# Performance work log

Hardware: AMD Instinct MI355X
Metric: run time of the kernel (lower is better)

Reference implementation:

```python
import jax, jax.numpy as jnp
import numpy as np

N, IN, OUT, T = 131072, 256, 256, 8

def setup_inputs() -> dict:
    key = jax.random.key(0)
    k1, k2, k3, k4 = jax.random.split(key, 4)
    x = jax.random.normal(k1, (N, IN), dtype=jnp.float32)
    type_vec = jnp.sort(jax.random.randint(k2, (N,), 0, T, dtype=jnp.int64))
    weight = jax.random.normal(k3, (T, IN, OUT), dtype=jnp.float32) * (1.0 / np.sqrt(IN))
    bias = jax.random.normal(k4, (T, OUT), dtype=jnp.float32) * 0.01
    return {"x": x, "type_vec": type_vec, "weight": weight, "bias": bias}

def reference(x, type_vec, weight, bias):
    # HeteroLinear fused forward: out[i] = x[i] @ weight[type_vec[i]] + bias[type_vec[i]]
    # Loop over the small fixed set of types (T=8); mask-accumulate keeps memory at O(N*OUT).
    num_types = weight.shape[0]
    out = jnp.zeros((x.shape[0], weight.shape[2]), dtype=x.dtype)
    for t in range(num_types):
        mask = (type_vec == t)[:, None]  # [N,1]
        out = out + jnp.where(mask, x @ weight[t] + bias[t], jnp.zeros((), x.dtype))
    return out
```

## Files before the change

kernel.cpp:

```cpp
#include <hip/hip_runtime.h>
#include <hip/hip_bf16.h>


#define NROWS 131072
#define KD 256
#define ND 256
#define BM 256
#define NBLK (NROWS / BM)

typedef __attribute__((ext_vector_type(8))) short short8;
typedef __attribute__((ext_vector_type(4))) float f32x4;
typedef __attribute__((ext_vector_type(4))) float flt4;

typedef __attribute__((address_space(3))) unsigned int lds_u32_t;
typedef __attribute__((address_space(1))) unsigned int glb_u32_t;

__device__ inline unsigned short f2bf(float f) {
    unsigned int u = __float_as_uint(f);
    u += 0x7FFFu + ((u >> 16) & 1u);
    return (unsigned short)(u >> 16);
}

__global__ __launch_bounds__(256) void prep_weights(const float* __restrict__ w,
                                                    unsigned short* __restrict__ wT) {
    __shared__ unsigned short L[8][264];
    const int t  = blockIdx.x >> 5;
    const int k0 = (blockIdx.x & 31) * 8;
    const int tid = threadIdx.x;

    #pragma unroll
    for (int i = 0; i < 2; ++i) {
        int idx = i * 256 + tid;
        int kr  = idx >> 6;
        int nq  = idx & 63;
        const flt4* src = (const flt4*)(w + ((size_t)t * 256 + k0 + kr) * 256);
        flt4 v = src[nq];
        #pragma unroll
        for (int j = 0; j < 4; ++j) L[kr][nq * 4 + j] = f2bf(v[j]);
    }
    __syncthreads();

    int n = tid;
    short8 v;
    #pragma unroll
    for (int j = 0; j < 8; ++j) v[j] = (short)L[j][n];
    *(short8*)(wT + ((size_t)t * 256 + n) * 256 + k0) = v;
}

__global__ __launch_bounds__(512) void hetero_gemm(
        const float* __restrict__ x, const int* __restrict__ tv,
        const unsigned short* __restrict__ wT, const float* __restrict__ bias,
        float* __restrict__ out) {
    __shared__ short Bs[BM * KD];

    const int tid  = threadIdx.x;
    const int lane = tid & 63;
    const int wv   = tid >> 6;
    const int cl   = lane & 15;
    const int kg   = lane >> 4;
    const int r0   = blockIdx.x * BM;
    const int rw   = r0 + wv * 32;

    const int tmin = tv[r0];
    const int tmax = tv[r0 + BM - 1];
    const int ty0  = tv[rw + cl];
    const int ty1  = tv[rw + 16 + cl];
    const int s    = cl & 7;

    const float* xr0 = x + (size_t)(rw + cl) * KD + kg * 8;
    const float* xr1 = x + (size_t)(rw + 16 + cl) * KD + kg * 8;

    for (int t = tmin; t <= tmax; ++t) {
        if (t > tmin) __syncthreads();

        {
            const unsigned short* Wt = wT + (size_t)t * (KD * ND);
            #pragma unroll
            for (int rnd = 0; rnd < 16; ++rnd) {
                int i   = rnd * 512 + tid;
                int col = i >> 5;
                int c   = i & 31;
                int sc  = c ^ (col & 7);
                const unsigned short* gp = Wt + col * KD + sc * 8;
                __builtin_amdgcn_global_load_lds(
                    (const glb_u32_t*)gp,
                    (lds_u32_t*)((char*)Bs + (size_t)(rnd * 512 + wv * 64) * 16),
                    16, 0, 0);
            }
        }
        __syncthreads();

        #pragma unroll
        for (int half = 0; half < 2; ++half) {
            const int c0 = half * 128;

            f32x4 zero = {0.f, 0.f, 0.f, 0.f};
            f32x4 acc[2][8];
            #pragma unroll
            for (int m = 0; m < 2; ++m)
                #pragma unroll
                for (int n = 0; n < 8; ++n) acc[m][n] = zero;

            f32x4 xbA[4], xbB[4];
            xbA[0] = *(const f32x4*)(xr0);
            xbA[1] = *(const f32x4*)(xr0 + 4);
            xbA[2] = *(const f32x4*)(xr1);
            xbA[3] = *(const f32x4*)(xr1 + 4);
            xbB[0] = *(const f32x4*)(xr0 + 32);
            xbB[1] = *(const f32x4*)(xr0 + 36);
            xbB[2] = *(const f32x4*)(xr1 + 32);
            xbB[3] = *(const f32x4*)(xr1 + 36);

            auto step = [&](f32x4 (&xb)[4], int ks) {
                short8 a[2];
                #pragma unroll
                for (int m = 0; m < 2; ++m) {
                    #pragma unroll
                    for (int j = 0; j < 4; ++j) {
                        a[m][j]     = (short)f2bf(xb[2 * m][j]);
                        a[m][4 + j] = (short)f2bf(xb[2 * m + 1][j]);
                    }
                }
                if (ks + 2 < 8) {
                    xb[0] = *(const f32x4*)(xr0 + (ks + 2) * 32);
                    xb[1] = *(const f32x4*)(xr0 + (ks + 2) * 32 + 4);
                    xb[2] = *(const f32x4*)(xr1 + (ks + 2) * 32);
                    xb[3] = *(const f32x4*)(xr1 + (ks + 2) * 32 + 4);
                }
                #pragma unroll
                for (int n = 0; n < 8; ++n) {
                    int lc = c0 + n * 16 + cl;
                    int kc = ((ks << 2) | kg) ^ s;
                    short8 b = *(const short8*)((char*)Bs + (size_t)lc * 512 + (kc << 4));
                    acc[0][n] = __builtin_amdgcn_mfma_f32_16x16x32_bf16(b, a[0], acc[0][n], 0, 0, 0);
                    acc[1][n] = __builtin_amdgcn_mfma_f32_16x16x32_bf16(b, a[1], acc[1][n], 0, 0, 0);
                }
            };
            step(xbA, 0); step(xbB, 1); step(xbA, 2); step(xbB, 3);
            step(xbA, 4); step(xbB, 5); step(xbA, 6); step(xbB, 7);

            #pragma unroll
            for (int m = 0; m < 2; ++m) {
                int tym = (m == 0) ? ty0 : ty1;
                if (tym == t) {
                    float* orow = out + (size_t)(rw + m * 16 + cl) * ND + c0 + kg * 4;
                    #pragma unroll
                    for (int n = 0; n < 8; ++n) {
                        f32x4 bv = *(const f32x4*)(bias + (size_t)t * ND + c0 + n * 16 + kg * 4);
                        *(f32x4*)(orow + n * 16) = acc[m][n] + bv;
                    }
                }
            }
        }
    }
}

extern "C" void kernel_launch(void* const* d_in, const int* in_sizes, int n_in,
                              void* d_out, int out_size, void* d_ws, size_t ws_size,
                              hipStream_t stream) {
    const float* x    = (const float*)d_in[0];
    const int*   tv   = (const int*)d_in[1];
    const float* w    = (const float*)d_in[2];
    const float* bias = (const float*)d_in[3];
    float* out = (float*)d_out;
    unsigned short* wT = (unsigned short*)d_ws;

    prep_weights<<<dim3(256), dim3(256), 0, stream>>>(w, wT);
    hetero_gemm<<<dim3(NBLK), dim3(512), 0, stream>>>(x, tv, wT, bias, out);
}
```

Baseline: 66.80 us.

## Split output columns across workgroups with 128-row tiles and swizzled block mapping

Each workgroup now covers 128 rows and one 128-column half of the output with 4 waves, instead of 256 rows and both halves with 8 waves. The LDS weight tile drops to 64KB, so more workgroups can be resident per CU. A blockIdx remap spreads neighbouring row groups across XCDs. The bf16 conversion now uses the library intrinsic. The trade-off is that each x row is read and converted twice, once per column half, and weight tiles are reloaded more often overall.

New measurement: 91.09 us. 36.4% more time.

```diff
diff --git a/kernel.cpp b/kernel.cpp
--- a/kernel.cpp
+++ b/kernel.cpp
@@ -5,8 +5,9 @@
 #define NROWS 131072
 #define KD 256
 #define ND 256
-#define BM 256
-#define NBLK (NROWS / BM)
+#define BR 128
+#define NRG (NROWS / BR)
+#define NBLK (NRG * 2)
 
 typedef __attribute__((ext_vector_type(8))) short short8;
 typedef __attribute__((ext_vector_type(4))) float f32x4;
@@ -16,9 +17,7 @@
 typedef __attribute__((address_space(1))) unsigned int glb_u32_t;
 
 __device__ inline unsigned short f2bf(float f) {
-    unsigned int u = __float_as_uint(f);
-    u += 0x7FFFu + ((u >> 16) & 1u);
-    return (unsigned short)(u >> 16);
+    return __bfloat16_as_ushort(__float2bfloat16(f));
 }
 
 __global__ __launch_bounds__(256) void prep_weights(const float* __restrict__ w,
@@ -47,22 +46,25 @@
     *(short8*)(wT + ((size_t)t * 256 + n) * 256 + k0) = v;
 }
 
-__global__ __launch_bounds__(512) void hetero_gemm(
+__global__ __launch_bounds__(256) void hetero_gemm(
         const float* __restrict__ x, const int* __restrict__ tv,
         const unsigned short* __restrict__ wT, const float* __restrict__ bias,
         float* __restrict__ out) {
-    __shared__ short Bs[BM * KD];
+    __shared__ short Bs[128 * KD];
 
     const int tid  = threadIdx.x;
     const int lane = tid & 63;
     const int wv   = tid >> 6;
     const int cl   = lane & 15;
     const int kg   = lane >> 4;
-    const int r0   = blockIdx.x * BM;
+    const int wgid = (blockIdx.x & 7) * (NBLK / 8) + (blockIdx.x >> 3);
+    const int rg   = wgid >> 1;
+    const int c0   = (wgid & 1) * 128;
+    const int r0   = rg * BR;
     const int rw   = r0 + wv * 32;
 
     const int tmin = tv[r0];
-    const int tmax = tv[r0 + BM - 1];
+    const int tmax = tv[r0 + BR - 1];
     const int ty0  = tv[rw + cl];
     const int ty1  = tv[rw + 16 + cl];
     const int s    = cl & 7;
@@ -77,78 +79,73 @@
             const unsigned short* Wt = wT + (size_t)t * (KD * ND);
             #pragma unroll
             for (int rnd = 0; rnd < 16; ++rnd) {
-                int i   = rnd * 512 + tid;
-                int col = i >> 5;
+                int i   = rnd * 256 + tid;
+                int lc  = i >> 5;
                 int c   = i & 31;
-                int sc  = c ^ (col & 7);
-                const unsigned short* gp = Wt + col * KD + sc * 8;
+                int sc  = c ^ (lc & 7);
+                const unsigned short* gp = Wt + (size_t)(c0 + lc) * KD + sc * 8;
                 __builtin_amdgcn_global_load_lds(
                     (const glb_u32_t*)gp,
-                    (lds_u32_t*)((char*)Bs + (size_t)(rnd * 512 + wv * 64) * 16),
+                    (lds_u32_t*)((char*)Bs + (size_t)(rnd * 256 + wv * 64) * 16),
                     16, 0, 0);
             }
         }
         __syncthreads();
 
+        f32x4 zero = {0.f, 0.f, 0.f, 0.f};
+        f32x4 acc[2][8];
         #pragma unroll
-        for (int half = 0; half < 2; ++half) {
-            const int c0 = half * 128;
+        for (int m = 0; m < 2; ++m)
+            #pragma unroll
+            for (int n = 0; n < 8; ++n) acc[m][n] = zero;
 
-            f32x4 zero = {0.f, 0.f, 0.f, 0.f};
-            f32x4 acc[2][8];
+        f32x4 xbA[4], xbB[4];
+        xbA[0] = *(const f32x4*)(xr0);
+        xbA[1] = *(const f32x4*)(xr0 + 4);
+        xbA[2] = *(const f32x4*)(xr1);
+        xbA[3] = *(const f32x4*)(xr1 + 4);
+        xbB[0] = *(const f32x4*)(xr0 + 32);
+        xbB[1] = *(const f32x4*)(xr0 + 36);
+        xbB[2] = *(const f32x4*)(xr1 + 32);
+        xbB[3] = *(const f32x4*)(xr1 + 36);
+
+        auto step = [&](f32x4 (&xb)[4], int ks) {
+            short8 a[2];
             #pragma unroll
-            for (int m = 0; m < 2; ++m)
+            for (int m = 0; m < 2; ++m) {
                 #pragma unroll
-                for (int n = 0; n < 8; ++n) acc[m][n] = zero;
+                for (int j = 0; j < 4; ++j) {
+                    a[m][j]     = (short)f2bf(xb[2 * m][j]);
+                    a[m][4 + j] = (short)f2bf(xb[2 * m + 1][j]);
+                }
+            }
+            if (ks + 2 < 8) {
+                xb[0] = *(const f32x4*)(xr0 + (ks + 2) * 32);
+                xb[1] = *(const f32x4*)(xr0 + (ks + 2) * 32 + 4);
+                xb[2] = *(const f32x4*)(xr1 + (ks + 2) * 32);
+                xb[3] = *(const f32x4*)(xr1 + (ks + 2) * 32 + 4);
+            }
+            #pragma unroll
+            for (int n = 0; n < 8; ++n) {
+                int lc = n * 16 + cl;
+                int kc = ((ks << 2) | kg) ^ s;
+                short8 b = *(const short8*)((char*)Bs + (size_t)lc * 512 + (kc << 4));
+                acc[0][n] = __builtin_amdgcn_mfma_f32_16x16x32_bf16(b, a[0], acc[0][n], 0, 0, 0);
+                acc[1][n] = __builtin_amdgcn_mfma_f32_16x16x32_bf16(b, a[1], acc[1][n], 0, 0, 0);
+            }
+        };
+        step(xbA, 0); step(xbB, 1); step(xbA, 2); step(xbB, 3);
+        step(xbA, 4); step(xbB, 5); step(xbA, 6); step(xbB, 7);
 
-            f32x4 xbA[4], xbB[4];
-            xbA[0] = *(const f32x4*)(xr0);
-            xbA[1] = *(const f32x4*)(xr0 + 4);
-            xbA[2] = *(const f32x4*)(xr1);
-            xbA[3] = *(const f32x4*)(xr1 + 4);
-            xbB[0] = *(const f32x4*)(xr0 + 32);
-            xbB[1] = *(const f32x4*)(xr0 + 36);
-            xbB[2] = *(const f32x4*)(xr1 + 32);
-            xbB[3] = *(const f32x4*)(xr1 + 36);
-
-            auto step = [&](f32x4 (&xb)[4], int ks) {
-                short8 a[2];
-                #pragma unroll
-                for (int m = 0; m < 2; ++m) {
-                    #pragma unroll
-                    for (int j = 0; j < 4; ++j) {
-                        a[m][j]     = (short)f2bf(xb[2 * m][j]);
-                        a[m][4 + j] = (short)f2bf(xb[2 * m + 1][j]);
-                    }
-                }
-                if (ks + 2 < 8) {
-                    xb[0] = *(const f32x4*)(xr0 + (ks + 2) * 32);
-                    xb[1] = *(const f32x4*)(xr0 + (ks + 2) * 32 + 4);
-                    xb[2] = *(const f32x4*)(xr1 + (ks + 2) * 32);
-                    xb[3] = *(const f32x4*)(xr1 + (ks + 2) * 32 + 4);
-                }
+        #pragma unroll
+        for (int m = 0; m < 2; ++m) {
+            int tym = (m == 0) ? ty0 : ty1;
+            if (tym == t) {
+                float* orow = out + (size_t)(rw + m * 16 + cl) * ND + c0 + kg * 4;
                 #pragma unroll
                 for (int n = 0; n < 8; ++n) {
-                    int lc = c0 + n * 16 + cl;
-                    int kc = ((ks << 2) | kg) ^ s;
-                    short8 b = *(const short8*)((char*)Bs + (size_t)lc * 512 + (kc << 4));
-                    acc[0][n] = __builtin_amdgcn_mfma_f32_16x16x32_bf16(b, a[0], acc[0][n], 0, 0, 0);
-                    acc[1][n] = __builtin_amdgcn_mfma_f32_16x16x32_bf16(b, a[1], acc[1][n], 0, 0, 0);
-                }
-            };
-            step(xbA, 0); step(xbB, 1); step(xbA, 2); step(xbB, 3);
-            step(xbA, 4); step(xbB, 5); step(xbA, 6); step(xbB, 7);
-
-            #pragma unroll
-            for (int m = 0; m < 2; ++m) {
-                int tym = (m == 0) ? ty0 : ty1;
-                if (tym == t) {
-                    float* orow = out + (size_t)(rw + m * 16 + cl) * ND + c0 + kg * 4;
-                    #pragma unroll
-                    for (int n = 0; n < 8; ++n) {
-                        f32x4 bv = *(const f32x4*)(bias + (size_t)t * ND + c0 + n * 16 + kg * 4);
-                        *(f32x4*)(orow + n * 16) = acc[m][n] + bv;
-                    }
+                    f32x4 bv = *(const f32x4*)(bias + (size_t)t * ND + c0 + n * 16 + kg * 4);
+                    *(f32x4*)(orow + n * 16) = acc[m][n] + bv;
                 }
             }
         }
@@ -166,5 +163,5 @@
     unsigned short* wT = (unsigned short*)d_ws;
 
     prep_weights<<<dim3(256), dim3(256), 0, stream>>>(w, wT);
-    hetero_gemm<<<dim3(NBLK), dim3(512), 0, stream>>>(x, tv, wT, bias, out);
+    hetero_gemm<<<dim3(NBLK), dim3(256), 0, stream>>>(x, tv, wT, bias, out);
 }
```

## Split output columns across blocks and stage x tiles in LDS via async DMA

Applied to the files above, without the earlier changes.

Doubles the grid so each block computes one 128-column half of the output for its 256-row group, halving the weight tile kept in LDS. The x rows are now loaded with global_load_lds into a double-buffered, XOR-swizzled LDS area, using explicit vmcnt/lgkmcnt waits to overlap the next k-step's loads with the MFMAs. Block indices are remapped so that blocks sharing a row group are spread across XCDs. This is meant to raise occupancy and hide the latency of x loads. In exchange, every row of x is read twice from global memory, and the code depends on hand-written waitcnt and inline asm being correct.

New measurement: 69.86 us. 4.6% more time.

```diff
diff --git a/kernel.cpp b/kernel.cpp
--- a/kernel.cpp
+++ b/kernel.cpp
@@ -6,7 +6,7 @@
 #define KD 256
 #define ND 256
 #define BM 256
-#define NBLK (NROWS / BM)
+#define NBLK ((NROWS / BM) * 2)
 
 typedef __attribute__((ext_vector_type(8))) short short8;
 typedef __attribute__((ext_vector_type(4))) float f32x4;
@@ -19,6 +19,12 @@
     unsigned int u = __float_as_uint(f);
     u += 0x7FFFu + ((u >> 16) & 1u);
     return (unsigned short)(u >> 16);
+}
+
+__device__ inline f32x4 lds_read_b128(unsigned addr) {
+    f32x4 v;
+    asm volatile("ds_read_b128 %0, %1" : "=v"(v) : "v"(addr));
+    return v;
 }
 
 __global__ __launch_bounds__(256) void prep_weights(const float* __restrict__ w,
@@ -51,14 +57,18 @@
         const float* __restrict__ x, const int* __restrict__ tv,
         const unsigned short* __restrict__ wT, const float* __restrict__ bias,
         float* __restrict__ out) {
-    __shared__ short Bs[BM * KD];
+    __shared__ short Bs[128 * KD];
+    __shared__ float Xs[2 * 8 * 32 * 32];
 
     const int tid  = threadIdx.x;
     const int lane = tid & 63;
     const int wv   = tid >> 6;
     const int cl   = lane & 15;
     const int kg   = lane >> 4;
-    const int r0   = blockIdx.x * BM;
+    const int wgid = (blockIdx.x & 7) * (NBLK / 8) + (blockIdx.x >> 3);
+    const int rg   = wgid >> 1;
+    const int c0   = (wgid & 1) * 128;
+    const int r0   = rg * BM;
     const int rw   = r0 + wv * 32;
 
     const int tmin = tv[r0];
@@ -67,8 +77,20 @@
     const int ty1  = tv[rw + 16 + cl];
     const int s    = cl & 7;
 
-    const float* xr0 = x + (size_t)(rw + cl) * KD + kg * 8;
-    const float* xr1 = x + (size_t)(rw + 16 + cl) * KD + kg * 8;
+    const unsigned xwbase = (unsigned)(uintptr_t)&Xs[wv * 1024];
+
+    auto DMA_X = [&](int ks) {
+        const int buf = ks & 1;
+        #pragma unroll
+        for (int i = 0; i < 4; ++i) {
+            const float* gp = x + (size_t)(rw + 8 * i + (lane >> 3)) * KD
+                                + ks * 32 + (((lane & 7) ^ (lane >> 3)) << 2);
+            __builtin_amdgcn_global_load_lds(
+                (const glb_u32_t*)gp,
+                (lds_u32_t*)&Xs[(buf * 8 + wv) * 1024 + i * 256],
+                16, 0, 0);
+        }
+    };
 
     for (int t = tmin; t <= tmax; ++t) {
         if (t > tmin) __syncthreads();
@@ -76,79 +98,71 @@
         {
             const unsigned short* Wt = wT + (size_t)t * (KD * ND);
             #pragma unroll
-            for (int rnd = 0; rnd < 16; ++rnd) {
-                int i   = rnd * 512 + tid;
-                int col = i >> 5;
-                int c   = i & 31;
-                int sc  = c ^ (col & 7);
-                const unsigned short* gp = Wt + col * KD + sc * 8;
+            for (int rnd = 0; rnd < 8; ++rnd) {
+                int i  = rnd * 512 + tid;
+                int lc = i >> 5;
+                int c  = i & 31;
+                int sc = c ^ (lc & 7);
+                const unsigned short* gp = Wt + (size_t)(c0 + lc) * KD + sc * 8;
                 __builtin_amdgcn_global_load_lds(
                     (const glb_u32_t*)gp,
                     (lds_u32_t*)((char*)Bs + (size_t)(rnd * 512 + wv * 64) * 16),
                     16, 0, 0);
             }
         }
+        DMA_X(0); DMA_X(1);
         __syncthreads();
 
+        f32x4 zero = {0.f, 0.f, 0.f, 0.f};
+        f32x4 acc[2][8];
         #pragma unroll
-        for (int half = 0; half < 2; ++half) {
-            const int c0 = half * 128;
+        for (int m = 0; m < 2; ++m)
+            #pragma unroll
+            for (int n = 0; n < 8; ++n) acc[m][n] = zero;
 
-            f32x4 zero = {0.f, 0.f, 0.f, 0.f};
-            f32x4 acc[2][8];
-            #pragma unroll
-            for (int m = 0; m < 2; ++m)
-                #pragma unroll
-                for (int n = 0; n < 8; ++n) acc[m][n] = zero;
+        #define KSTEP(ks)                                                          \
+        {                                                                          \
+            if ((ks) < 7) asm volatile("s_waitcnt vmcnt(4)" ::: "memory");         \
+            else          asm volatile("s_waitcnt vmcnt(0)" ::: "memory");         \
+            __builtin_amdgcn_sched_barrier(0);                                     \
+            const unsigned sb = xwbase + (((ks) & 1) << 15);                       \
+            f32x4 v00 = lds_read_b128(sb + cl * 128 + (((2 * kg + 0) ^ s) << 4));  \
+            f32x4 v01 = lds_read_b128(sb + cl * 128 + (((2 * kg + 1) ^ s) << 4));  \
+            f32x4 v10 = lds_read_b128(sb + (16 + cl) * 128 + (((2 * kg + 0) ^ s) << 4)); \
+            f32x4 v11 = lds_read_b128(sb + (16 + cl) * 128 + (((2 * kg + 1) ^ s) << 4)); \
+            asm volatile("s_waitcnt lgkmcnt(0)" ::: "memory");                     \
+            __builtin_amdgcn_sched_barrier(0);                                     \
+            if ((ks) < 6) DMA_X((ks) + 2);           \
+            short8 a0, a1;                                                         \
+            _Pragma("unroll")                                                      \
+            for (int j = 0; j < 4; ++j) {                                          \
+                a0[j]     = (short)f2bf(v00[j]);                                   \
+                a0[4 + j] = (short)f2bf(v01[j]);                                   \
+                a1[j]     = (short)f2bf(v10[j]);                                   \
+                a1[4 + j] = (short)f2bf(v11[j]);                                   \
+            }                                                                      \
+            _Pragma("unroll")                                                      \
+            for (int n = 0; n < 8; ++n) {                                          \
+                int lc = n * 16 + cl;                                              \
+                int kc = (((ks) << 2) | kg) ^ s;                                   \
+                short8 b = *(const short8*)((char*)Bs + (size_t)lc * 512 + (kc << 4)); \
+                acc[0][n] = __builtin_amdgcn_mfma_f32_16x16x32_bf16(b, a0, acc[0][n], 0, 0, 0); \
+                acc[1][n] = __builtin_amdgcn_mfma_f32_16x16x32_bf16(b, a1, acc[1][n], 0, 0, 0); \
+            }                                                                      \
+        }
+        KSTEP(0) KSTEP(1) KSTEP(2) KSTEP(3)
+        KSTEP(4) KSTEP(5) KSTEP(6) KSTEP(7)
+        #undef KSTEP
 
-            f32x4 xbA[4], xbB[4];
-            xbA[0] = *(const f32x4*)(xr0);
-            xbA[1] = *(const f32x4*)(xr0 + 4);
-            xbA[2] = *(const f32x4*)(xr1);
-            xbA[3] = *(const f32x4*)(xr1 + 4);
-            xbB[0] = *(const f32x4*)(xr0 + 32);
-            xbB[1] = *(const f32x4*)(xr0 + 36);
-            xbB[2] = *(const f32x4*)(xr1 + 32);
-            xbB[3] = *(const f32x4*)(xr1 + 36);
-
-            auto step = [&](f32x4 (&xb)[4], int ks) {
-                short8 a[2];
-                #pragma unroll
-                for (int m = 0; m < 2; ++m) {
-                    #pragma unroll
-                    for (int j = 0; j < 4; ++j) {
-                        a[m][j]     = (short)f2bf(xb[2 * m][j]);
-                        a[m][4 + j] = (short)f2bf(xb[2 * m + 1][j]);
-                    }
-                }
-                if (ks + 2 < 8) {
-                    xb[0] = *(const f32x4*)(xr0 + (ks + 2) * 32);
-                    xb[1] = *(const f32x4*)(xr0 + (ks + 2) * 32 + 4);
-                    xb[2] = *(const f32x4*)(xr1 + (ks + 2) * 32);
-                    xb[3] = *(const f32x4*)(xr1 + (ks + 2) * 32 + 4);
-                }
+        #pragma unroll
+        for (int m = 0; m < 2; ++m) {
+            int tym = (m == 0) ? ty0 : ty1;
+            if (tym == t) {
+                float* orow = out + (size_t)(rw + m * 16 + cl) * ND + c0 + kg * 4;
                 #pragma unroll
                 for (int n = 0; n < 8; ++n) {
-                    int lc = c0 + n * 16 + cl;
-                    int kc = ((ks << 2) | kg) ^ s;
-                    short8 b = *(const short8*)((char*)Bs + (size_t)lc * 512 + (kc << 4));
-                    acc[0][n] = __builtin_amdgcn_mfma_f32_16x16x32_bf16(b, a[0], acc[0][n], 0, 0, 0);
-                    acc[1][n] = __builtin_amdgcn_mfma_f32_16x16x32_bf16(b, a[1], acc[1][n], 0, 0, 0);
-                }
-            };
-            step(xbA, 0); step(xbB, 1); step(xbA, 2); step(xbB, 3);
-            step(xbA, 4); step(xbB, 5); step(xbA, 6); step(xbB, 7);
-
-            #pragma unroll
-            for (int m = 0; m < 2; ++m) {
-                int tym = (m == 0) ? ty0 : ty1;
-                if (tym == t) {
-                    float* orow = out + (size_t)(rw + m * 16 + cl) * ND + c0 + kg * 4;
-                    #pragma unroll
-                    for (int n = 0; n < 8; ++n) {
-                        f32x4 bv = *(const f32x4*)(bias + (size_t)t * ND + c0 + n * 16 + kg * 4);
-                        *(f32x4*)(orow + n * 16) = acc[m][n] + bv;
-                    }
+                    f32x4 bv = *(const f32x4*)(bias + (size_t)t * ND + c0 + n * 16 + kg * 4);
+                    *(f32x4*)(orow + n * 16) = acc[m][n] + bv;
                 }
             }
         }
```
